# Kernel optimization log

Measured on AMD Instinct MI355X. Metric: run time of the kernel, lower is better.

The kernel has to match this reference:

```python
import jax, jax.numpy as jnp
import numpy as np

B, S, D, H = 4, 2048, 512, 8
HD = D // H


def setup_inputs() -> dict:
    key = jax.random.key(0)
    ks = jax.random.split(key, 12)
    x = jax.random.normal(ks[0], (B, S, D), dtype=jnp.float32)
    docking_scores = jax.random.uniform(ks[1], (B, S), dtype=jnp.float32)
    mask = jax.random.randint(ks[2], (B, S), 0, 2).astype(jnp.bool_)
    s = 0.02
    Wq = jax.random.normal(ks[3], (D, D), dtype=jnp.float32) * s
    bq = jnp.zeros((D,), dtype=jnp.float32)
    Wk = jax.random.normal(ks[4], (D, D), dtype=jnp.float32) * s
    bk = jnp.zeros((D,), dtype=jnp.float32)
    Wv = jax.random.normal(ks[5], (D, D), dtype=jnp.float32) * s
    bv = jnp.zeros((D,), dtype=jnp.float32)
    Wo = jax.random.normal(ks[6], (D, D), dtype=jnp.float32) * s
    bo = jnp.zeros((D,), dtype=jnp.float32)
    alpha = jnp.float32(0.5)
    beta = jnp.float32(0.5)
    return {"x": x, "docking_scores": docking_scores, "mask": mask,
            "Wq": Wq, "bq": bq, "Wk": Wk, "bk": bk, "Wv": Wv, "bv": bv,
            "Wo": Wo, "bo": bo, "alpha": alpha, "beta": beta}


def reference(x, docking_scores, mask, Wq, bq, Wk, bk, Wv, bv, Wo, bo, alpha, beta):
    # daa_type == ATTENTION: attention + docking-score blend (alpha unused here).
    b, s, d = x.shape
    # zero docking scores at padded positions; shape (B, S, 1)
    ds = jnp.where(mask[..., None], docking_scores[..., None], 0.0)
    def proj(W, bias):
        return (jnp.einsum('bsd,ed->bse', x, W) + bias).reshape(b, s, H, HD).transpose(0, 2, 1, 3)
    Q = proj(Wq, bq)  # (B, H, S, HD)
    K = proj(Wk, bk)
    V = proj(Wv, bv)
    scores = jnp.einsum('bhqd,bhkd->bhqk', Q, K) / jnp.sqrt(jnp.float32(HD))
    scores = jnp.where(mask[:, None, None, :], scores, -jnp.inf)  # key-padding mask
    attn = jax.nn.softmax(scores, axis=-1)  # (B, H, S, S)
    # docking blend: (B,1,S,1) broadcasts over heads and key dim (faithful to torch expand)
    attn = (1.0 - beta) * attn + beta * ds[:, None, :, :]
    ctx = jnp.einsum('bhqk,bhkd->bhqd', attn, V)
    ctx = ctx.transpose(0, 2, 1, 3).reshape(b, s, d)
    return jnp.einsum('bsd,od->bso', ctx, Wo) + bo
```

## Files before the change

kernel.cpp:

```cpp
#include <hip/hip_runtime.h>
#include <hip/hip_bf16.h>

#define B_ 4
#define S_ 2048
#define D_ 512
#define H_ 8
#define HD_ 64

typedef unsigned int uint;
typedef unsigned short ushort_t;
typedef __attribute__((ext_vector_type(4))) float f32x4;
typedef __attribute__((ext_vector_type(16))) float f32x16;
typedef __attribute__((ext_vector_type(8))) short bf16x8;

#if __has_builtin(__builtin_amdgcn_exp2f)
#define EXP2F __builtin_amdgcn_exp2f
#else
#define EXP2F exp2f
#endif

__device__ __forceinline__ float bf2f(unsigned short u){ union{uint i;float f;}c; c.i = (uint)u<<16; return c.f; }
__device__ __forceinline__ unsigned short f2bf(float f){
    __hip_bfloat16 h = __float2bfloat16(f);
    return *reinterpret_cast<unsigned short*>(&h);
}

__device__ __forceinline__ void gload16(const unsigned short* g, const ushort_t* l){
    __builtin_amdgcn_global_load_lds(
        (const __attribute__((address_space(1))) unsigned int*)g,
        (__attribute__((address_space(3))) unsigned int*)l, 16, 0, 0);
}

__global__ __launch_bounds__(256) void convert_all(
    const float* __restrict__ x,
    const float* __restrict__ Wq, const float* __restrict__ Wk,
    const float* __restrict__ Wv, const float* __restrict__ Wo,
    const int* __restrict__ mask,
    ushort_t* __restrict__ xb, ushort_t* __restrict__ Wqkvb, ushort_t* __restrict__ Wob,
    float* __restrict__ mbg)
{
    const int NX = 1048576;
    const int NW = 65536;
    const int total = NX + 4 * NW;
    for (int i = blockIdx.x * 256 + threadIdx.x; i < total; i += gridDim.x * 256) {
        const float* src; ushort_t* dst; int so, dofs;
        if (i < NX) { src = x; so = i; dst = xb; dofs = i; }
        else if (i < NX + 3 * NW) {
            int j = i - NX;
            if (j < NW)          { src = Wq; so = j; }
            else if (j < 2 * NW) { src = Wk; so = j - NW; }
            else                 { src = Wv; so = j - 2 * NW; }
            dst = Wqkvb; dofs = j;
        } else { int k = i - NX - 3 * NW; src = Wo; so = k; dst = Wob; dofs = k; }
        float4 v = ((const float4*)src)[so];
        ushort4 u;
        u.x = f2bf(v.x); u.y = f2bf(v.y); u.z = f2bf(v.z); u.w = f2bf(v.w);
        ((ushort4*)dst)[dofs] = u;
    }
    for (int i = blockIdx.x * 256 + threadIdx.x; i < 2048; i += gridDim.x * 256) {
        int4 mv = ((const int4*)mask)[i];
        float4 o;
        o.x = mv.x ? 0.f : -1e30f;
        o.y = mv.y ? 0.f : -1e30f;
        o.z = mv.z ? 0.f : -1e30f;
        o.w = mv.w ? 0.f : -1e30f;
        ((float4*)mbg)[i] = o;
    }
}

template<int MODE>
__global__ __launch_bounds__(256) void gemm_mfma(
    const ushort_t* __restrict__ A, const ushort_t* __restrict__ Bw,
    const float* __restrict__ b0, const float* __restrict__ b1, const float* __restrict__ b2,
    ushort_t* __restrict__ O0, ushort_t* __restrict__ O1, ushort_t* __restrict__ O2,
    float* __restrict__ Of)
{
    __shared__ __align__(16) unsigned char smem[34816];
    ushort_t* sA = (ushort_t*)smem;
    ushort_t* sB = sA + 8192;

    const int t = threadIdx.x, w = t >> 6, l = t & 63, g = l >> 4, c = l & 15;
    const int wm = w >> 1, wn = w & 1;
    const int row0 = blockIdx.y * 128, col0 = blockIdx.x * 128;

    const ushort_t* aSrc[4]; const ushort_t* bSrc[4];
    ushort_t* aDst[4]; ushort_t* bDst[4];
    #pragma unroll
    for (int i = 0; i < 4; ++i) {
        int cc = i * 256 + t;
        int row = cc >> 3, slot = (cc & 7) ^ (row & 7);
        aSrc[i] = A  + (size_t)(row0 + row) * 512 + slot * 8;
        bSrc[i] = Bw + (size_t)(col0 + row) * 512 + slot * 8;
        aDst[i] = sA + (i * 256 + w * 64) * 8;
        bDst[i] = sB + (i * 256 + w * 64) * 8;
    }

    f32x4 acc[4][4];
    #pragma unroll
    for (int mi = 0; mi < 4; ++mi)
        #pragma unroll
        for (int ni = 0; ni < 4; ++ni) acc[mi][ni] = (f32x4)0.f;

    for (int ks = 0; ks < 8; ++ks) {
        #pragma unroll
        for (int i = 0; i < 4; ++i) {
            gload16(aSrc[i], aDst[i]);
            gload16(bSrc[i], bDst[i]);
        }
        __syncthreads();
        #pragma unroll
        for (int kh = 0; kh < 2; ++kh) {
            bf16x8 af[4], bfv[4];
            const int sw = (((kh << 2) | g) ^ (c & 7)) << 3;
            #pragma unroll
            for (int mi = 0; mi < 4; ++mi)
                af[mi] = *(const bf16x8*)&sA[(wm * 64 + mi * 16 + c) * 64 + sw];
            #pragma unroll
            for (int ni = 0; ni < 4; ++ni)
                bfv[ni] = *(const bf16x8*)&sB[(wn * 64 + ni * 16 + c) * 64 + sw];
            #pragma unroll
            for (int mi = 0; mi < 4; ++mi)
                #pragma unroll
                for (int ni = 0; ni < 4; ++ni)
                    acc[mi][ni] = __builtin_amdgcn_mfma_f32_16x16x32_bf16(af[mi], bfv[ni], acc[mi][ni], 0, 0, 0);
        }
        #pragma unroll
        for (int i = 0; i < 4; ++i) { aSrc[i] += 64; bSrc[i] += 64; }
        __syncthreads();
    }

    if (MODE == 1) {
        #pragma unroll
        for (int mi = 0; mi < 4; ++mi)
            #pragma unroll
            for (int ni = 0; ni < 4; ++ni) {
                int n = col0 + wn * 64 + ni * 16 + c;
                float bias = b0[n];
                #pragma unroll
                for (int r = 0; r < 4; ++r)
                    Of[(size_t)(row0 + wm * 64 + mi * 16 + 4 * g + r) * 512 + n] =
                        acc[mi][ni][r] + bias;
            }
    } else {
        const int which = col0 >> 9;
        const float* bias = which == 0 ? b0 : (which == 1 ? b1 : b2);
        ushort_t (*Cl)[136] = (ushort_t(*)[136])smem;
        if (which < 2) {
            #pragma unroll
            for (int mi = 0; mi < 4; ++mi)
                #pragma unroll
                for (int ni = 0; ni < 4; ++ni) {
                    int n = wn * 64 + ni * 16 + c;
                    float bb = bias[(col0 & 511) + n];
                    #pragma unroll
                    for (int r = 0; r < 4; ++r)
                        Cl[wm * 64 + mi * 16 + 4 * g + r][n] = f2bf(acc[mi][ni][r] + bb);
                }
        } else {
            #pragma unroll
            for (int mi = 0; mi < 4; ++mi)
                #pragma unroll
                for (int ni = 0; ni < 4; ++ni) {
                    int n = wn * 64 + ni * 16 + c;
                    float bb = bias[(col0 & 511) + n];
                    #pragma unroll
                    for (int r = 0; r < 4; ++r)
                        Cl[n][wm * 64 + mi * 16 + 4 * g + r] = f2bf(acc[mi][ni][r] + bb);
                }
        }
        __syncthreads();
        const int r = t >> 1, half = t & 1;
        const int b = row0 >> 11;
        if (which < 2) {
            ushort_t* Out = which == 0 ? O0 : O1;
            int s = (row0 & 2047) + r;
            int e = (col0 & 511) + half * 64;
            int h = e >> 6;
            ushort_t* dst = Out + (((size_t)(b * 8 + h) * 2048 + s) << 6);
            #pragma unroll
            for (int j = 0; j < 8; ++j)
                *(bf16x8*)(dst + j * 8) = *(const bf16x8*)&Cl[r][half * 64 + j * 8];
        } else {
            int e = (col0 & 511) + r;
            int h = e >> 6, d = e & 63;
            int s0 = (row0 & 2047) + half * 64;
            ushort_t* dst = O2 + ((size_t)(b * 8 + h) * 64 + d) * 2048 + s0;
            #pragma unroll
            for (int j = 0; j < 8; ++j)
                *(bf16x8*)(dst + j * 8) = *(const bf16x8*)&Cl[r][half * 64 + j * 8];
        }
    }
}

__global__ __launch_bounds__(256) void vsum2(
    const __hip_bfloat16* __restrict__ Vt, float* __restrict__ Vsum)
{
    const int row = blockIdx.x * 4 + (threadIdx.x >> 6);
    const int l = threadIdx.x & 63;
    const unsigned short* p = (const unsigned short*)Vt + (size_t)row * S_;
    float s = 0.f;
    #pragma unroll
    for (int i = 0; i < 4; ++i) {
        uint4 u = *(const uint4*)(p + i * 512 + l * 8);
        s += bf2f((unsigned short)(u.x & 0xffff)) + bf2f((unsigned short)(u.x >> 16));
        s += bf2f((unsigned short)(u.y & 0xffff)) + bf2f((unsigned short)(u.y >> 16));
        s += bf2f((unsigned short)(u.z & 0xffff)) + bf2f((unsigned short)(u.z >> 16));
        s += bf2f((unsigned short)(u.w & 0xffff)) + bf2f((unsigned short)(u.w >> 16));
    }
    #pragma unroll
    for (int m = 1; m < 64; m <<= 1) s += __shfl_xor(s, m);
    if (l == 0) Vsum[row] = s;
}

__global__ __launch_bounds__(256, 2) void attn_mfma(
    const __hip_bfloat16* __restrict__ Qb, const __hip_bfloat16* __restrict__ Kb,
    const __hip_bfloat16* __restrict__ Vt, const float* __restrict__ Vsum,
    const float* __restrict__ dock, const int* __restrict__ mask,
    const float* __restrict__ mbg, const float* __restrict__ beta_p,
    ushort_t* __restrict__ ctxb)
{
    __shared__ __align__(16) unsigned char smem[35328];
    ushort_t* Kbuf = (ushort_t*)smem;
    ushort_t* Vbuf = (ushort_t*)(smem + 16384);

    const int flat = blockIdx.x;
    const int xcd = flat & 7, idx = flat >> 3;
    const int bh = ((idx >> 4) << 3) + xcd;
    const int qtile = idx & 15;
    const int b = bh >> 3, h8 = bh & 7;
    const int t = threadIdx.x, w = t >> 6, lam = t & 63;
    const int lq = lam & 31, hf = lam >> 5;
    const int q0 = qtile * 128 + w * 32;
    const int qg = q0 + lq;
    const float beta = beta_p[0];
    const ushort_t* Kp = (const ushort_t*)Kb + (size_t)bh * S_ * HD_;
    const ushort_t* Vp = (const ushort_t*)Vt + (size_t)bh * HD_ * S_;
    const float* mbp = mbg + b * S_;

    int koff[2], voff[2];
    const ushort_t* kdst[2]; const ushort_t* vdst[2];
    {
        const int srow = t >> 3, sslot = t & 7;
        #pragma unroll
        for (int ch = 0; ch < 2; ++ch) {
            int row = ch * 32 + srow;
            int sl = (sslot ^ (row & 7)) * 8;
            koff[ch] = row * 64 + sl;
            voff[ch] = row * 2048 + sl;
            kdst[ch] = Kbuf + (ch * 256 + w * 64) * 8;
            vdst[ch] = Vbuf + (ch * 256 + w * 64) * 8;
        }
    }
#define STAGE(PAR, K0N) do {                                                    \
    _Pragma("unroll")                                                           \
    for (int ch = 0; ch < 2; ++ch) {                                            \
        gload16(Kp + (size_t)(K0N) * 64 + koff[ch], kdst[ch] + (PAR) * 4096);   \
        gload16(Vp + (K0N) + voff[ch],              vdst[ch] + (PAR) * 4096);   \
    }                                                                           \
} while (0)

    STAGE(0, 0);

    bf16x8 qf[4];
    #pragma unroll
    for (int hd = 0; hd < 4; ++hd)
        qf[hd] = *(const bf16x8*)((const ushort_t*)Qb +
                 ((size_t)bh * S_ + qg) * HD_ + hd * 16 + hf * 8);

    f32x16 cacc[2];
    cacc[0] = (f32x16)0.f;
    cacc[1] = (f32x16)0.f;
    float l_ = 0.f;
    const float CSC = 0.18033688011112042f;

    __syncthreads();

    for (int k0 = 0, par = 0; k0 < S_; k0 += 64, par ^= 1) {
        if (k0 + 64 < S_) STAGE(par ^ 1, k0 + 64);
        const ushort_t* KB = Kbuf + par * 4096;
        const ushort_t* VB = Vbuf + par * 4096;

        f32x16 sacc[2];
        sacc[0] = (f32x16)0.f;
        sacc[1] = (f32x16)0.f;
        __builtin_amdgcn_s_setprio(1);
        #pragma unroll
        for (int kt2 = 0; kt2 < 2; ++kt2) {
            const int krow = kt2 * 32 + lq;
            const ushort_t* kr = KB + krow * 64;
            const int krs = krow & 7;
            #pragma unroll
            for (int hd = 0; hd < 4; ++hd) {
                bf16x8 kf = *(const bf16x8*)(kr + ((((hd << 1) | hf) ^ krs) << 3));
                sacc[kt2] = __builtin_amdgcn_mfma_f32_32x32x16_bf16(kf, qf[hd], sacc[kt2], 0, 0, 0);
            }
        }
        __builtin_amdgcn_s_setprio(0);

        float p[2][16];
        #pragma unroll
        for (int kt2 = 0; kt2 < 2; ++kt2) {
            #pragma unroll
            for (int qd = 0; qd < 4; ++qd) {
                float4 mb = *(const float4*)(mbp + k0 + kt2 * 32 + qd * 8 + hf * 4);
                float pv0 = EXP2F(fmaf(sacc[kt2][qd * 4 + 0], CSC, mb.x));
                float pv1 = EXP2F(fmaf(sacc[kt2][qd * 4 + 1], CSC, mb.y));
                float pv2 = EXP2F(fmaf(sacc[kt2][qd * 4 + 2], CSC, mb.z));
                float pv3 = EXP2F(fmaf(sacc[kt2][qd * 4 + 3], CSC, mb.w));
                p[kt2][qd * 4 + 0] = pv0; p[kt2][qd * 4 + 1] = pv1;
                p[kt2][qd * 4 + 2] = pv2; p[kt2][qd * 4 + 3] = pv3;
                l_ += pv0 + pv1 + pv2 + pv3;
            }
        }

        __builtin_amdgcn_s_setprio(1);
        #pragma unroll
        for (int kt2 = 0; kt2 < 2; ++kt2) {
            #pragma unroll
            for (int ks = 0; ks < 2; ++ks) {
                bf16x8 pf;
                #pragma unroll
                for (int m = 0; m < 8; ++m)
                    pf[m] = (short)f2bf(p[kt2][ks * 8 + m]);
                const int gB = (kt2 << 2) + (ks << 1);
                #pragma unroll
                for (int dt = 0; dt < 2; ++dt) {
                    const int vrow = dt * 32 + lq;
                    const int vrs = vrow & 7;
                    const ushort_t* vr = VB + vrow * 64;
                    uint2 lo = *(const uint2*)(vr + (((gB    ) ^ vrs) << 3) + (hf << 2));
                    uint2 hi = *(const uint2*)(vr + (((gB + 1) ^ vrs) << 3) + (hf << 2));
                    union { bf16x8 v; uint4 u; } cv;
                    cv.u = make_uint4(lo.x, lo.y, hi.x, hi.y);
                    cacc[dt] = __builtin_amdgcn_mfma_f32_32x32x16_bf16(cv.v, pf, cacc[dt], 0, 0, 0);
                }
            }
        }
        __builtin_amdgcn_s_setprio(0);
        __syncthreads();
    }
#undef STAGE

    l_ += __shfl_xor(l_, 32);

    __syncthreads();

    float (*ctxl)[32][68] = (float(*)[32][68])smem;
    {
        float w1 = (1.f - beta) / l_;
        float dq = (mask[b * S_ + qg] ? dock[b * S_ + qg] : 0.f) * beta;
        #pragma unroll
        for (int dt = 0; dt < 2; ++dt)
            #pragma unroll
            for (int qd = 0; qd < 4; ++qd) {
                int d0 = dt * 32 + qd * 8 + hf * 4;
                float4 vs = *(const float4*)(Vsum + bh * 64 + d0);
                float4 o;
                o.x = cacc[dt][qd * 4 + 0] * w1 + dq * vs.x;
                o.y = cacc[dt][qd * 4 + 1] * w1 + dq * vs.y;
                o.z = cacc[dt][qd * 4 + 2] * w1 + dq * vs.z;
                o.w = cacc[dt][qd * 4 + 3] * w1 + dq * vs.w;
                *(float4*)&ctxl[w][lq][d0] = o;
            }
    }
    asm volatile("s_waitcnt lgkmcnt(0)" ::: "memory");
    __builtin_amdgcn_sched_barrier(0);
    {
        const int qloc = lam >> 1, half = lam & 1;
        const int qg2 = q0 + qloc;
        ushort_t* cp = ctxb + ((size_t)(b * 2048 + qg2)) * 512 + h8 * 64 + half * 32;
        #pragma unroll
        for (int j = 0; j < 4; ++j) {
            float4 v0 = *(const float4*)&ctxl[w][qloc][half * 32 + j * 8];
            float4 v1 = *(const float4*)&ctxl[w][qloc][half * 32 + j * 8 + 4];
            bf16x8 u;
            u[0] = (short)f2bf(v0.x); u[1] = (short)f2bf(v0.y);
            u[2] = (short)f2bf(v0.z); u[3] = (short)f2bf(v0.w);
            u[4] = (short)f2bf(v1.x); u[5] = (short)f2bf(v1.y);
            u[6] = (short)f2bf(v1.z); u[7] = (short)f2bf(v1.w);
            *(bf16x8*)(cp + j * 8) = u;
        }
    }
}

extern "C" void kernel_launch(void* const* d_in, const int* in_sizes, int n_in,
                              void* d_out, int out_size, void* d_ws, size_t ws_size,
                              hipStream_t stream)
{
    const float* x    = (const float*)d_in[0];
    const float* dock = (const float*)d_in[1];
    const int*   mask = (const int*)d_in[2];
    const float* Wq   = (const float*)d_in[3];
    const float* bq   = (const float*)d_in[4];
    const float* Wk   = (const float*)d_in[5];
    const float* bk   = (const float*)d_in[6];
    const float* Wv   = (const float*)d_in[7];
    const float* bv   = (const float*)d_in[8];
    const float* Wo   = (const float*)d_in[9];
    const float* bo   = (const float*)d_in[10];
    const float* beta = (const float*)d_in[12];
    float* out = (float*)d_out;

    const size_t nqkv = (size_t)B_ * H_ * S_ * HD_;
    ushort_t* xb    = (ushort_t*)d_ws;
    ushort_t* Qb    = xb + nqkv;
    ushort_t* Kb    = Qb + nqkv;
    ushort_t* Vt    = Kb + nqkv;
    ushort_t* Wqkvb = Vt + nqkv;
    ushort_t* Wob   = Wqkvb + 1536 * 512;
    float*    Vsum  = (float*)(Wob + 512 * 512);
    float*    mbg   = Vsum + 2048;
    ushort_t* ctxb  = xb;

    convert_all<<<1280, 256, 0, stream>>>(x, Wq, Wk, Wv, Wo, mask, xb, Wqkvb, Wob, mbg);
    gemm_mfma<0><<<dim3(12, 64), 256, 0, stream>>>(xb, Wqkvb, bq, bk, bv, Qb, Kb, Vt, nullptr);
    vsum2<<<512, 256, 0, stream>>>((const __hip_bfloat16*)Vt, Vsum);
    attn_mfma<<<512, 256, 0, stream>>>(
        (const __hip_bfloat16*)Qb, (const __hip_bfloat16*)Kb, (const __hip_bfloat16*)Vt,
        Vsum, dock, mask, mbg, beta, ctxb);
    gemm_mfma<1><<<dim3(4, 64), 256, 0, stream>>>(ctxb, Wob, bo, nullptr, nullptr,
                                                  nullptr, nullptr, nullptr, out);
}
```

Measured before the change: 122.3 us.

## Double query tile per wave and switch K/V staging to register prefetch

Each wave now handles 64 queries as two 32-row MFMA tiles that share every K and V fragment read from LDS, halving LDS traffic per FLOP. The grid shrinks from 512 to 256 blocks with launch bounds set to one block per SM. K/V staging moves from direct global-to-LDS loads to register prefetch with a new 16-slot XOR swizzle, and the epilogue stages bf16 instead of fp32. Only 256 blocks on a many-CU GPU plus higher register pressure risk lower occupancy and less latency hiding.

```diff
diff --git a/kernel.cpp b/kernel.cpp
--- a/kernel.cpp
+++ b/kernel.cpp
@@ -212,174 +212,201 @@
     if (l == 0) Vsum[row] = s;
 }
 
-__global__ __launch_bounds__(256, 2) void attn_mfma(
+__global__ __launch_bounds__(256, 1) void attn_mfma(
     const __hip_bfloat16* __restrict__ Qb, const __hip_bfloat16* __restrict__ Kb,
     const __hip_bfloat16* __restrict__ Vt, const float* __restrict__ Vsum,
     const float* __restrict__ dock, const int* __restrict__ mask,
     const float* __restrict__ mbg, const float* __restrict__ beta_p,
     ushort_t* __restrict__ ctxb)
 {
-    __shared__ __align__(16) unsigned char smem[35328];
+    __shared__ __align__(16) unsigned char smem[36864];
     ushort_t* Kbuf = (ushort_t*)smem;
     ushort_t* Vbuf = (ushort_t*)(smem + 16384);
 
     const int flat = blockIdx.x;
     const int xcd = flat & 7, idx = flat >> 3;
-    const int bh = ((idx >> 4) << 3) + xcd;
-    const int qtile = idx & 15;
+    const int bh = ((idx >> 3) << 3) | xcd;
+    const int qtile = idx & 7;
     const int b = bh >> 3, h8 = bh & 7;
     const int t = threadIdx.x, w = t >> 6, lam = t & 63;
     const int lq = lam & 31, hf = lam >> 5;
-    const int q0 = qtile * 128 + w * 32;
-    const int qg = q0 + lq;
+    const int q0 = qtile * 256 + w * 64;
     const float beta = beta_p[0];
     const ushort_t* Kp = (const ushort_t*)Kb + (size_t)bh * S_ * HD_;
     const ushort_t* Vp = (const ushort_t*)Vt + (size_t)bh * HD_ * S_;
     const float* mbp = mbg + b * S_;
 
-    int koff[2], voff[2];
-    const ushort_t* kdst[2]; const ushort_t* vdst[2];
+    const int srow = t >> 2, squad = t & 3;
+    const int sx = ((srow & 7) << 1) | ((srow >> 3) & 1);
+    int wof[4];
+    #pragma unroll
+    for (int i = 0; i < 4; ++i)
+        wof[i] = srow * 64 + ((((squad << 2) | i) ^ sx) << 2);
+
+    const int xr = ((lq & 7) << 1) | ((lq >> 3) & 1);
+
+    bf16x8 qf[2][4];
+    #pragma unroll
+    for (int qt2 = 0; qt2 < 2; ++qt2)
+        #pragma unroll
+        for (int hd = 0; hd < 4; ++hd)
+            qf[qt2][hd] = *(const bf16x8*)((const ushort_t*)Qb +
+                ((size_t)bh * S_ + q0 + qt2 * 32 + lq) * HD_ + hd * 16 + hf * 8);
+
+    f32x16 cacc[2][2];
+    cacc[0][0] = (f32x16)0.f; cacc[0][1] = (f32x16)0.f;
+    cacc[1][0] = (f32x16)0.f; cacc[1][1] = (f32x16)0.f;
+    float l_[2] = {0.f, 0.f};
+    const float CSC = 0.18033688011112042f;
+
     {
-        const int srow = t >> 3, sslot = t & 7;
-        #pragma unroll
-        for (int ch = 0; ch < 2; ++ch) {
-            int row = ch * 32 + srow;
-            int sl = (sslot ^ (row & 7)) * 8;
-            koff[ch] = row * 64 + sl;
-            voff[ch] = row * 2048 + sl;
-            kdst[ch] = Kbuf + (ch * 256 + w * 64) * 8;
-            vdst[ch] = Vbuf + (ch * 256 + w * 64) * 8;
-        }
-    }
-#define STAGE(PAR, K0N) do {                                                    \
-    _Pragma("unroll")                                                           \
-    for (int ch = 0; ch < 2; ++ch) {                                            \
-        gload16(Kp + (size_t)(K0N) * 64 + koff[ch], kdst[ch] + (PAR) * 4096);   \
-        gload16(Vp + (K0N) + voff[ch],              vdst[ch] + (PAR) * 4096);   \
-    }                                                                           \
-} while (0)
-
-    STAGE(0, 0);
-
-    bf16x8 qf[4];
-    #pragma unroll
-    for (int hd = 0; hd < 4; ++hd)
-        qf[hd] = *(const bf16x8*)((const ushort_t*)Qb +
-                 ((size_t)bh * S_ + qg) * HD_ + hd * 16 + hf * 8);
-
-    f32x16 cacc[2];
-    cacc[0] = (f32x16)0.f;
-    cacc[1] = (f32x16)0.f;
-    float l_ = 0.f;
-    const float CSC = 0.18033688011112042f;
-
+        uint4 kg0 = *(const uint4*)(Kp + (size_t)srow * 64 + squad * 16);
+        uint4 kg1 = *(const uint4*)(Kp + (size_t)srow * 64 + squad * 16 + 8);
+        uint4 vg0 = *(const uint4*)(Vp + (size_t)srow * 2048 + squad * 16);
+        uint4 vg1 = *(const uint4*)(Vp + (size_t)srow * 2048 + squad * 16 + 8);
+        *(uint2*)(Kbuf + wof[0]) = make_uint2(kg0.x, kg0.y);
+        *(uint2*)(Kbuf + wof[1]) = make_uint2(kg0.z, kg0.w);
+        *(uint2*)(Kbuf + wof[2]) = make_uint2(kg1.x, kg1.y);
+        *(uint2*)(Kbuf + wof[3]) = make_uint2(kg1.z, kg1.w);
+        *(uint2*)(Vbuf + wof[0]) = make_uint2(vg0.x, vg0.y);
+        *(uint2*)(Vbuf + wof[1]) = make_uint2(vg0.z, vg0.w);
+        *(uint2*)(Vbuf + wof[2]) = make_uint2(vg1.x, vg1.y);
+        *(uint2*)(Vbuf + wof[3]) = make_uint2(vg1.z, vg1.w);
+    }
     __syncthreads();
 
-    for (int k0 = 0, par = 0; k0 < S_; k0 += 64, par ^= 1) {
-        if (k0 + 64 < S_) STAGE(par ^ 1, k0 + 64);
-        const ushort_t* KB = Kbuf + par * 4096;
-        const ushort_t* VB = Vbuf + par * 4096;
-
-        f32x16 sacc[2];
-        sacc[0] = (f32x16)0.f;
-        sacc[1] = (f32x16)0.f;
+    for (int k0 = 0; k0 < S_; k0 += 64) {
+        const int par = (k0 >> 6) & 1;
+        const ushort_t* KBp = Kbuf + par * 4096;
+        const ushort_t* VBp = Vbuf + par * 4096;
+        const bool pre = (k0 + 64 < S_);
+
+        uint4 kg0, kg1, vg0, vg1;
+        if (pre) {
+            kg0 = *(const uint4*)(Kp + (size_t)(k0 + 64 + srow) * 64 + squad * 16);
+            kg1 = *(const uint4*)(Kp + (size_t)(k0 + 64 + srow) * 64 + squad * 16 + 8);
+            vg0 = *(const uint4*)(Vp + (size_t)srow * 2048 + k0 + 64 + squad * 16);
+            vg1 = *(const uint4*)(Vp + (size_t)srow * 2048 + k0 + 64 + squad * 16 + 8);
+        }
+        float4 mb[2][4];
+        #pragma unroll
+        for (int kt2 = 0; kt2 < 2; ++kt2)
+            #pragma unroll
+            for (int qd = 0; qd < 4; ++qd)
+                mb[kt2][qd] = *(const float4*)(mbp + k0 + kt2 * 32 + qd * 8 + hf * 4);
+
+        f32x16 sacc[2][2];
+        sacc[0][0] = (f32x16)0.f; sacc[0][1] = (f32x16)0.f;
+        sacc[1][0] = (f32x16)0.f; sacc[1][1] = (f32x16)0.f;
         __builtin_amdgcn_s_setprio(1);
         #pragma unroll
         for (int kt2 = 0; kt2 < 2; ++kt2) {
-            const int krow = kt2 * 32 + lq;
-            const ushort_t* kr = KB + krow * 64;
-            const int krs = krow & 7;
+            const ushort_t* kr = KBp + (kt2 * 32 + lq) * 64;
             #pragma unroll
             for (int hd = 0; hd < 4; ++hd) {
-                bf16x8 kf = *(const bf16x8*)(kr + ((((hd << 1) | hf) ^ krs) << 3));
-                sacc[kt2] = __builtin_amdgcn_mfma_f32_32x32x16_bf16(kf, qf[hd], sacc[kt2], 0, 0, 0);
+                uint2 lo = *(const uint2*)(kr + ((((hd << 2) | (hf << 1)) ^ xr) << 2));
+                uint2 hi = *(const uint2*)(kr + ((((hd << 2) | (hf << 1) | 1) ^ xr) << 2));
+                union { bf16x8 v; uint4 u; } kf;
+                kf.u = make_uint4(lo.x, lo.y, hi.x, hi.y);
+                sacc[0][kt2] = __builtin_amdgcn_mfma_f32_32x32x16_bf16(kf.v, qf[0][hd], sacc[0][kt2], 0, 0, 0);
+                sacc[1][kt2] = __builtin_amdgcn_mfma_f32_32x32x16_bf16(kf.v, qf[1][hd], sacc[1][kt2], 0, 0, 0);
             }
         }
         __builtin_amdgcn_s_setprio(0);
 
-        float p[2][16];
-        #pragma unroll
-        for (int kt2 = 0; kt2 < 2; ++kt2) {
-            #pragma unroll
-            for (int qd = 0; qd < 4; ++qd) {
-                float4 mb = *(const float4*)(mbp + k0 + kt2 * 32 + qd * 8 + hf * 4);
-                float pv0 = EXP2F(fmaf(sacc[kt2][qd * 4 + 0], CSC, mb.x));
-                float pv1 = EXP2F(fmaf(sacc[kt2][qd * 4 + 1], CSC, mb.y));
-                float pv2 = EXP2F(fmaf(sacc[kt2][qd * 4 + 2], CSC, mb.z));
-                float pv3 = EXP2F(fmaf(sacc[kt2][qd * 4 + 3], CSC, mb.w));
-                p[kt2][qd * 4 + 0] = pv0; p[kt2][qd * 4 + 1] = pv1;
-                p[kt2][qd * 4 + 2] = pv2; p[kt2][qd * 4 + 3] = pv3;
-                l_ += pv0 + pv1 + pv2 + pv3;
-            }
+        float p[2][2][16];
+        #pragma unroll
+        for (int qt2 = 0; qt2 < 2; ++qt2) {
+            float ps = 0.f;
+            #pragma unroll
+            for (int kt2 = 0; kt2 < 2; ++kt2)
+                #pragma unroll
+                for (int qd = 0; qd < 4; ++qd) {
+                    float4 m4 = mb[kt2][qd];
+                    float p0 = EXP2F(fmaf(sacc[qt2][kt2][qd * 4 + 0], CSC, m4.x));
+                    float p1 = EXP2F(fmaf(sacc[qt2][kt2][qd * 4 + 1], CSC, m4.y));
+                    float p2 = EXP2F(fmaf(sacc[qt2][kt2][qd * 4 + 2], CSC, m4.z));
+                    float p3 = EXP2F(fmaf(sacc[qt2][kt2][qd * 4 + 3], CSC, m4.w));
+                    p[qt2][kt2][qd * 4 + 0] = p0; p[qt2][kt2][qd * 4 + 1] = p1;
+                    p[qt2][kt2][qd * 4 + 2] = p2; p[qt2][kt2][qd * 4 + 3] = p3;
+                    ps += p0 + p1 + p2 + p3;
+                }
+            l_[qt2] += ps;
         }
 
         __builtin_amdgcn_s_setprio(1);
         #pragma unroll
-        for (int kt2 = 0; kt2 < 2; ++kt2) {
+        for (int kt2 = 0; kt2 < 2; ++kt2)
             #pragma unroll
             for (int ks = 0; ks < 2; ++ks) {
-                bf16x8 pf;
-                #pragma unroll
-                for (int m = 0; m < 8; ++m)
-                    pf[m] = (short)f2bf(p[kt2][ks * 8 + m]);
-                const int gB = (kt2 << 2) + (ks << 1);
+                bf16x8 pf0, pf1;
+                #pragma unroll
+                for (int m = 0; m < 8; ++m) {
+                    pf0[m] = (short)f2bf(p[0][kt2][ks * 8 + m]);
+                    pf1[m] = (short)f2bf(p[1][kt2][ks * 8 + m]);
+                }
                 #pragma unroll
                 for (int dt = 0; dt < 2; ++dt) {
-                    const int vrow = dt * 32 + lq;
-                    const int vrs = vrow & 7;
-                    const ushort_t* vr = VB + vrow * 64;
-                    uint2 lo = *(const uint2*)(vr + (((gB    ) ^ vrs) << 3) + (hf << 2));
-                    uint2 hi = *(const uint2*)(vr + (((gB + 1) ^ vrs) << 3) + (hf << 2));
-                    union { bf16x8 v; uint4 u; } cv;
-                    cv.u = make_uint4(lo.x, lo.y, hi.x, hi.y);
-                    cacc[dt] = __builtin_amdgcn_mfma_f32_32x32x16_bf16(cv.v, pf, cacc[dt], 0, 0, 0);
+                    const ushort_t* vr = VBp + (dt * 32 + lq) * 64;
+                    uint2 lo = *(const uint2*)(vr + (((8 * kt2 + 4 * ks + hf) ^ xr) << 2));
+                    uint2 hi = *(const uint2*)(vr + (((8 * kt2 + 4 * ks + 2 + hf) ^ xr) << 2));
+                    union { bf16x8 v; uint4 u; } vf;
+                    vf.u = make_uint4(lo.x, lo.y, hi.x, hi.y);
+                    cacc[0][dt] = __builtin_amdgcn_mfma_f32_32x32x16_bf16(vf.v, pf0, cacc[0][dt], 0, 0, 0);
+                    cacc[1][dt] = __builtin_amdgcn_mfma_f32_32x32x16_bf16(vf.v, pf1, cacc[1][dt], 0, 0, 0);
                 }
             }
-        }
         __builtin_amdgcn_s_setprio(0);
+
+        if (pre) {
+            ushort_t* KD = Kbuf + (par ^ 1) * 4096;
+            ushort_t* VD = Vbuf + (par ^ 1) * 4096;
+            *(uint2*)(KD + wof[0]) = make_uint2(kg0.x, kg0.y);
+            *(uint2*)(KD + wof[1]) = make_uint2(kg0.z, kg0.w);
+            *(uint2*)(KD + wof[2]) = make_uint2(kg1.x, kg1.y);
+            *(uint2*)(KD + wof[3]) = make_uint2(kg1.z, kg1.w);
+            *(uint2*)(VD + wof[0]) = make_uint2(vg0.x, vg0.y);
+            *(uint2*)(VD + wof[1]) = make_uint2(vg0.z, vg0.w);
+            *(uint2*)(VD + wof[2]) = make_uint2(vg1.x, vg1.y);
+            *(uint2*)(VD + wof[3]) = make_uint2(vg1.z, vg1.w);
+        }
         __syncthreads();
     }
-#undef STAGE
-
-    l_ += __shfl_xor(l_, 32);
+
+    l_[0] += __shfl_xor(l_[0], 32);
+    l_[1] += __shfl_xor(l_[1], 32);
 
     __syncthreads();
 
-    float (*ctxl)[32][68] = (float(*)[32][68])smem;
+    ushort_t* ctxl = (ushort_t*)smem;
+    #pragma unroll
+    for (int qt2 = 0; qt2 < 2; ++qt2) {
+        const int qg = q0 + qt2 * 32 + lq;
+        const float w1 = (1.f - beta) / l_[qt2];
+        const float dq = (mask[b * S_ + qg] ? dock[b * S_ + qg] : 0.f) * beta;
+        #pragma unroll
+        for (int dt = 0; dt < 2; ++dt)
+            #pragma unroll
+            for (int qd = 0; qd < 4; ++qd) {
+                const int d0 = dt * 32 + qd * 8 + hf * 4;
+                float4 vs = *(const float4*)(Vsum + bh * 64 + d0);
+                float o0 = cacc[qt2][dt][qd * 4 + 0] * w1 + dq * vs.x;
+                float o1 = cacc[qt2][dt][qd * 4 + 1] * w1 + dq * vs.y;
+                float o2 = cacc[qt2][dt][qd * 4 + 2] * w1 + dq * vs.z;
+                float o3 = cacc[qt2][dt][qd * 4 + 3] * w1 + dq * vs.w;
+                uint lo = (uint)f2bf(o0) | ((uint)f2bf(o1) << 16);
+                uint hi = (uint)f2bf(o2) | ((uint)f2bf(o3) << 16);
+                *(uint2*)(ctxl + (size_t)w * 4608 + (qt2 * 32 + lq) * 72 + d0) =
+                    make_uint2(lo, hi);
+            }
+    }
+    __syncthreads();
     {
-        float w1 = (1.f - beta) / l_;
-        float dq = (mask[b * S_ + qg] ? dock[b * S_ + qg] : 0.f) * beta;
-        #pragma unroll
-        for (int dt = 0; dt < 2; ++dt)
-            #pragma unroll
-            for (int qd = 0; qd < 4; ++qd) {
-                int d0 = dt * 32 + qd * 8 + hf * 4;
-                float4 vs = *(const float4*)(Vsum + bh * 64 + d0);
-                float4 o;
-                o.x = cacc[dt][qd * 4 + 0] * w1 + dq * vs.x;
-                o.y = cacc[dt][qd * 4 + 1] * w1 + dq * vs.y;
-                o.z = cacc[dt][qd * 4 + 2] * w1 + dq * vs.z;
-                o.w = cacc[dt][qd * 4 + 3] * w1 + dq * vs.w;
-                *(float4*)&ctxl[w][lq][d0] = o;
-            }
-    }
-    asm volatile("s_waitcnt lgkmcnt(0)" ::: "memory");
-    __builtin_amdgcn_sched_barrier(0);
-    {
-        const int qloc = lam >> 1, half = lam & 1;
-        const int qg2 = q0 + qloc;
-        ushort_t* cp = ctxb + ((size_t)(b * 2048 + qg2)) * 512 + h8 * 64 + half * 32;
-        #pragma unroll
-        for (int j = 0; j < 4; ++j) {
-            float4 v0 = *(const float4*)&ctxl[w][qloc][half * 32 + j * 8];
-            float4 v1 = *(const float4*)&ctxl[w][qloc][half * 32 + j * 8 + 4];
-            bf16x8 u;
-            u[0] = (short)f2bf(v0.x); u[1] = (short)f2bf(v0.y);
-            u[2] = (short)f2bf(v0.z); u[3] = (short)f2bf(v0.w);
-            u[4] = (short)f2bf(v1.x); u[5] = (short)f2bf(v1.y);
-            u[6] = (short)f2bf(v1.z); u[7] = (short)f2bf(v1.w);
-            *(bf16x8*)(cp + j * 8) = u;
-        }
+        ushort_t* cp = ctxb + ((size_t)(b * 2048 + q0 + lam)) * 512 + h8 * 64;
+        const ushort_t* rp = ctxl + (size_t)w * 4608 + lam * 72;
+        #pragma unroll
+        for (int j = 0; j < 8; ++j)
+            *(bf16x8*)(cp + j * 8) = *(const bf16x8*)(rp + j * 8);
     }
 }
 
@@ -415,7 +442,7 @@
     convert_all<<<1280, 256, 0, stream>>>(x, Wq, Wk, Wv, Wo, mask, xb, Wqkvb, Wob, mbg);
     gemm_mfma<0><<<dim3(12, 64), 256, 0, stream>>>(xb, Wqkvb, bq, bk, bv, Qb, Kb, Vt, nullptr);
     vsum2<<<512, 256, 0, stream>>>((const __hip_bfloat16*)Vt, Vsum);
-    attn_mfma<<<512, 256, 0, stream>>>(
+    attn_mfma<<<256, 256, 0, stream>>>(
         (const __hip_bfloat16*)Qb, (const __hip_bfloat16*)Kb, (const __hip_bfloat16*)Vt,
         Vsum, dock, mask, mbg, beta, ctxb);
     gemm_mfma<1><<<dim3(4, 64), 256, 0, stream>>>(ctxb, Wob, bo, nullptr, nullptr,
```

Result: no change. 123.1 us (+0.7%).
